# Kernel optimization log

Measured on AMD Instinct MI355X. Metric: run time of the kernel, lower is better.

## Reference

```python
import jax, jax.numpy as jnp
import numpy as np

B, D, E, K = 8192, 1024, 8, 2048  # tokens, dim, num_experts, k (per-expert capacity)


def setup_inputs() -> dict:
    key = jax.random.key(0)
    ks = jax.random.split(key, 5)
    x = jax.random.normal(ks[0], (B, D), dtype=jnp.float32)
    Wr = jax.random.normal(ks[1], (D, E), dtype=jnp.float32) * 0.02
    br = jnp.zeros((E,), jnp.float32)
    W1 = jax.random.normal(ks[2], (E, D, 4 * D), dtype=jnp.float32) * 0.02
    b1 = jnp.zeros((E, 4 * D), jnp.float32)
    W2 = jax.random.normal(ks[3], (E, 4 * D, D), dtype=jnp.float32) * 0.02
    b2 = jnp.zeros((E, D), jnp.float32)
    return {"x": x, "Wr": Wr, "br": br, "W1": W1, "b1": b1, "W2": W2, "b2": b2}


def _dispatch_weights(x, Wr, br):
    # Expert-choice routing: softmax over experts per token, each expert picks top-K tokens.
    gate = jax.nn.softmax(x @ Wr + br, axis=-1)          # [B, E]
    vals, idx = jax.lax.top_k(gate.T, K)                 # [E, K] each
    w = jnp.zeros((x.shape[0], E), x.dtype)
    w = w.at[idx.reshape(-1), jnp.repeat(jnp.arange(E), K)].set(vals.reshape(-1))
    # torch source builds dispatch_weights via .tolist(), detaching it from autograd
    return jax.lax.stop_gradient(w)                      # [B, E]


def reference(x, Wr, br, W1, b1, W2, b2):
    w = _dispatch_weights(x, Wr, br)                     # [B, E]
    mask = (w > 0).astype(x.dtype)                       # [B, E]
    xm = x[None, :, :] * mask.T[:, :, None]              # [E, B, D] (dense masked input, as in source)
    h = jax.nn.relu(jnp.einsum('ebd,edh->ebh', xm, W1) + b1[:, None, :])   # [E, B, 4D]
    y = jnp.einsum('ebh,ehd->ebd', h, W2) + b2[:, None, :]                 # [E, B, D]
    out = jnp.einsum('ebd,be->bd', y, w)                 # weighted combine over experts
    return out
```

## Files before the change

kernel.cpp:

```cpp
#include <hip/hip_runtime.h>
#include <hip/hip_bf16.h>

#define BTOK 8192
#define DDIM 1024
#define NEXP 8
#define KCAP 2048
#define HDIM 4096
#define MB ((size_t)1048576)

typedef __attribute__((ext_vector_type(4))) float f32x4;
typedef __attribute__((ext_vector_type(8))) short bf16x8;

__device__ __forceinline__ unsigned short f2bf(float f) {
    union { float f; unsigned u; } v; v.f = f;
    unsigned r = v.u + 0x7fffu + ((v.u >> 16) & 1u);
    return (unsigned short)(r >> 16);
}

typedef __attribute__((address_space(3))) unsigned int lds_u32;
typedef __attribute__((address_space(1))) const unsigned int glb_u32;
__device__ __forceinline__ void gl_lds16(const void* g, void* l) {
    __builtin_amdgcn_global_load_lds((glb_u32*)g, (lds_u32*)l, 16, 0, 0);
}

__global__ __launch_bounds__(256) void router_kernel(
    const float* __restrict__ x, const float* __restrict__ Wr,
    const float* __restrict__ br, float* __restrict__ gateT,
    unsigned short* __restrict__ xb) {
    __shared__ float wr_s[NEXP][DDIM];
    int t = threadIdx.x;
    for (int i = t; i < NEXP * DDIM; i += 256) {
        int e = i >> 10, d = i & 1023;
        wr_s[e][d] = Wr[d * NEXP + e];
    }
    __syncthreads();
    int wid = t >> 6, lane = t & 63;
    int b = blockIdx.x * 4 + wid;
    const float4* xr = (const float4*)(x + (size_t)b * DDIM);
    float4 xv[4];
#pragma unroll
    for (int j = 0; j < 4; j++) xv[j] = xr[j * 64 + lane];
#pragma unroll
    for (int j = 0; j < 4; j++) {
        short4 s;
        s.x = (short)f2bf(xv[j].x); s.y = (short)f2bf(xv[j].y);
        s.z = (short)f2bf(xv[j].z); s.w = (short)f2bf(xv[j].w);
        *(short4*)(xb + (size_t)b * DDIM + (j * 64 + lane) * 4) = s;
    }
    double acc[NEXP];
#pragma unroll
    for (int e = 0; e < NEXP; e++) {
        double a = 0.0;
#pragma unroll
        for (int j = 0; j < 4; j++) {
            float4 wv = ((const float4*)&wr_s[e][0])[j * 64 + lane];
            a += (double)xv[j].x * wv.x + (double)xv[j].y * wv.y
               + (double)xv[j].z * wv.z + (double)xv[j].w * wv.w;
        }
#pragma unroll
        for (int s = 1; s < 64; s <<= 1) a += __shfl_xor(a, s, 64);
        acc[e] = a + (double)br[e];
    }
    if (lane == 0) {
        double mx = acc[0];
#pragma unroll
        for (int e = 1; e < NEXP; e++) mx = fmax(mx, acc[e]);
        double p[NEXP]; double ssum = 0.0;
#pragma unroll
        for (int e = 0; e < NEXP; e++) { p[e] = exp(acc[e] - mx); ssum += p[e]; }
        double inv = 1.0 / ssum;
#pragma unroll
        for (int e = 0; e < NEXP; e++) gateT[e * BTOK + b] = (float)(p[e] * inv);
    }
}

__global__ __launch_bounds__(256) void select_kernel(
    const float* __restrict__ gateT, unsigned* __restrict__ meta) {
    int e = blockIdx.x, t = threadIdx.x;
    const float* g = gateT + e * BTOK;
    __shared__ unsigned hist[256];
    __shared__ unsigned sh_prefix;
    __shared__ int sh_rem;
    if (t == 0) { sh_prefix = 0; sh_rem = KCAP; }
    __syncthreads();
    for (int pass = 0; pass < 4; pass++) {
        int shift = 24 - pass * 8;
        hist[t] = 0;
        __syncthreads();
        unsigned pfx = sh_prefix;
        for (int i = t; i < BTOK; i += 256) {
            unsigned key = __float_as_uint(g[i]);
            if (pass == 0 || (key >> (shift + 8)) == pfx)
                atomicAdd(&hist[(key >> shift) & 255u], 1u);
        }
        __syncthreads();
        if (t == 0) {
            int rem = sh_rem, cum = 0, d = 0;
            for (int dd = 255; dd >= 0; dd--) {
                cum += (int)hist[dd];
                if (cum >= rem) { d = dd; break; }
            }
            sh_rem = rem - (cum - (int)hist[d]);
            sh_prefix = (pfx << 8) | (unsigned)d;
        }
        __syncthreads();
    }
    unsigned cutoff = sh_prefix;
    int cnt = 0;
    for (int i = t; i < BTOK; i += 256)
        if (__float_as_uint(g[i]) > cutoff) cnt++;
    __shared__ int red[256];
    red[t] = cnt; __syncthreads();
    for (int s = 128; s > 0; s >>= 1) { if (t < s) red[t] += red[t + s]; __syncthreads(); }
    if (t == 0) { meta[e] = cutoff; meta[NEXP + e] = (unsigned)red[0]; }
}

__global__ __launch_bounds__(256) void build_kernel(
    const float* __restrict__ gateT, const unsigned* __restrict__ meta,
    unsigned* __restrict__ cnt, int* __restrict__ idx_list, float* __restrict__ wt_list) {
    int e = blockIdx.y;
    int b = blockIdx.x * 256 + threadIdx.x;
    float gv = gateT[(size_t)e * BTOK + b];
    if (__float_as_uint(gv) > meta[e]) {
        unsigned pos = atomicAdd(&cnt[e], 1u);
        if (pos < KCAP) {
            idx_list[(size_t)e * KCAP + pos] = b;
            wt_list[(size_t)e * KCAP + pos] = gv;
        }
    }
}

__global__ __launch_bounds__(256) void tie_kernel(
    const float* __restrict__ gateT, const unsigned* __restrict__ meta,
    unsigned* __restrict__ cnt, int* __restrict__ idx_list, float* __restrict__ wt_list) {
    int e = blockIdx.x, t = threadIdx.x;
    unsigned cutoff = meta[e];
    int need = KCAP - (int)meta[NEXP + e];
    const float* g = gateT + (size_t)e * BTOK;
    __shared__ int pre[256];
    int base = t * 32;
    int c = 0;
    for (int j = 0; j < 32; j++) c += (__float_as_uint(g[base + j]) == cutoff) ? 1 : 0;
    pre[t] = c;
    __syncthreads();
    for (int s = 1; s < 256; s <<= 1) {
        int v = (t >= s) ? pre[t - s] : 0;
        __syncthreads();
        pre[t] += v;
        __syncthreads();
    }
    int rank = pre[t] - c;
    for (int j = 0; j < 32; j++) {
        float gv = g[base + j];
        if (__float_as_uint(gv) == cutoff) {
            if (rank < need) {
                unsigned pos = atomicAdd(&cnt[e], 1u);
                if (pos < KCAP) {
                    idx_list[(size_t)e * KCAP + pos] = base + j;
                    wt_list[(size_t)e * KCAP + pos] = gv;
                }
            }
            rank++;
        }
    }
}

__global__ __launch_bounds__(256) void invb_kernel(
    const int* __restrict__ idx_list, int* __restrict__ inv) {
    int i = blockIdx.x * 256 + threadIdx.x;
    int e = i >> 11, slot = i & (KCAP - 1);
    inv[(size_t)e * BTOK + idx_list[i]] = slot;
}

__global__ __launch_bounds__(256) void tcvt_kernel(
    const float* __restrict__ src, unsigned short* __restrict__ dst, int R, int C) {
    size_t zoff = (size_t)blockIdx.z * R * C;
    src += zoff; dst += zoff;
    __shared__ unsigned short tile[64][72];
    int c0 = blockIdx.x * 64, r0 = blockIdx.y * 64;
    int t = threadIdx.x;
    int cq = t & 15, rr = t >> 4;
#pragma unroll
    for (int ri = 0; ri < 4; ri++) {
        int r = ri * 16 + rr;
        float4 v = *(const float4*)(src + (size_t)(r0 + r) * C + c0 + cq * 4);
        tile[cq * 4 + 0][r] = f2bf(v.x);
        tile[cq * 4 + 1][r] = f2bf(v.y);
        tile[cq * 4 + 2][r] = f2bf(v.z);
        tile[cq * 4 + 3][r] = f2bf(v.w);
    }
    __syncthreads();
    int rq = t & 15, cc = t >> 4;
#pragma unroll
    for (int ci = 0; ci < 4; ci++) {
        int c = ci * 16 + cc;
        *(short4*)(dst + (size_t)(c0 + c) * R + r0 + rq * 4) = *(const short4*)&tile[c][rq * 4];
    }
}


#define ASLOT 4096
#define BSLOT 8192

__global__ __launch_bounds__(512, 4) void gemm1_kernel(
    const unsigned short* __restrict__ xb, const unsigned short* __restrict__ w1t,
    const float* __restrict__ b1, const int* __restrict__ idx_list,
    unsigned short* __restrict__ h) {
    int bid = blockIdx.x;
    int e = bid & 7, idx = bid >> 3;
    int m0 = (idx & 15) * 128, n0 = (idx >> 4) * 256;
    w1t      += (size_t)e * DDIM * HDIM;
    b1       += (size_t)e * HDIM;
    idx_list += (size_t)e * KCAP;
    h        += (size_t)e * KCAP * HDIM;
    __shared__ unsigned short As[3 * ASLOT];
    __shared__ unsigned short Bs[3 * BSLOT];
    __shared__ int toks[128];
    int t = threadIdx.x;
    if (t < 128) toks[t] = idx_list[m0 + t];
    __syncthreads();
    int w = t >> 6, lane = t & 63, l4 = lane >> 2;
    unsigned swz = (unsigned)(((lane & 3) ^ ((lane >> 3) & 3)) << 4);
    const char* pa  = (const char*)(xb + (size_t)toks[w * 16 + l4] * DDIM) + swz;
    const char* pb0 = (const char*)(w1t + (size_t)(n0 + w * 16 + l4) * DDIM) + swz;
    const char* pb1 = (const char*)(w1t + (size_t)(n0 + 128 + w * 16 + l4) * DDIM) + swz;
    unsigned short* da  = As + (w * 16) * 32;
    unsigned short* db0 = Bs + (w * 16) * 32;
    unsigned short* db1 = Bs + (128 + w * 16) * 32;
#define ST1(slot, koff) do {                                         \
    gl_lds16(pa  + (koff), da  + (slot) * ASLOT);                    \
    gl_lds16(pb0 + (koff), db0 + (slot) * BSLOT);                    \
    gl_lds16(pb1 + (koff), db1 + (slot) * BSLOT); } while (0)
    int wm = w >> 2, wn = w & 3;
    int fr = lane & 15, kg = lane >> 4;
    unsigned koffr = (unsigned)((kg ^ ((fr >> 1) & 3)) << 4);
    const int NT = DDIM / 32;
    f32x4 acc[4][4] = {};
    ST1(0, 0); ST1(1, 64);
    asm volatile("s_waitcnt vmcnt(3)" ::: "memory");
    __builtin_amdgcn_s_barrier();
    size_t ko = 128;
    int sw = 2, sr = 0;
    for (int kt = 0; kt < NT; kt++) {
        if (kt + 2 < NT) { ST1(sw, ko); ko += 64; }
        const char* ab = (const char*)As + sr * (ASLOT * 2);
        const char* bb = (const char*)Bs + sr * (BSLOT * 2);
        bf16x8 af[4], bf[4];
#pragma unroll
        for (int mf = 0; mf < 4; mf++)
            af[mf] = *(const bf16x8*)(ab + (wm * 64 + mf * 16 + fr) * 64 + koffr);
#pragma unroll
        for (int nf = 0; nf < 4; nf++)
            bf[nf] = *(const bf16x8*)(bb + (wn * 64 + nf * 16 + fr) * 64 + koffr);
        __builtin_amdgcn_s_setprio(1);
#pragma unroll
        for (int mf = 0; mf < 4; mf++)
#pragma unroll
            for (int nf = 0; nf < 4; nf++)
                acc[mf][nf] = __builtin_amdgcn_mfma_f32_16x16x32_bf16(
                    af[mf], bf[nf], acc[mf][nf], 0, 0, 0);
        __builtin_amdgcn_s_setprio(0);
        if (kt + 1 < NT) {
            if (kt + 2 < NT) asm volatile("s_waitcnt vmcnt(3)" ::: "memory");
            else             asm volatile("s_waitcnt vmcnt(0)" ::: "memory");
            __builtin_amdgcn_s_barrier();
        }
        sw = (sw == 2) ? 0 : sw + 1;
        sr = (sr == 2) ? 0 : sr + 1;
    }
#undef ST1
    int hi = lane >> 4;
#pragma unroll
    for (int nf = 0; nf < 4; nf++) {
        int col = n0 + wn * 64 + nf * 16 + fr;
        float bias = b1[col];
#pragma unroll
        for (int mf = 0; mf < 4; mf++) {
            int r0 = wm * 64 + mf * 16 + hi * 4;
#pragma unroll
            for (int r = 0; r < 4; r++) {
                float v = fmaxf(acc[mf][nf][r] + bias, 0.f);
                h[(size_t)(m0 + r0 + r) * HDIM + col] = f2bf(v);
            }
        }
    }
}

__global__ __launch_bounds__(512, 4) void gemm2y_kernel(
    const unsigned short* __restrict__ h, const unsigned short* __restrict__ w2t,
    const float* __restrict__ b2, const float* __restrict__ wt_list,
    float* __restrict__ yb) {
    int bid = blockIdx.x;
    int e = bid & 7, idx = bid >> 3;
    int m0 = (idx & 15) * 128, n0 = (idx >> 4) * 256;
    h       += (size_t)e * KCAP * HDIM;
    w2t     += (size_t)e * DDIM * HDIM;
    b2      += (size_t)e * DDIM;
    wt_list += (size_t)e * KCAP;
    yb      += (size_t)e * KCAP * DDIM;
    __shared__ unsigned short As[3 * ASLOT];
    __shared__ unsigned short Bs[3 * BSLOT];
    __shared__ float wts[128];
    int t = threadIdx.x;
    if (t < 128) wts[t] = wt_list[m0 + t];
    __syncthreads();
    int w = t >> 6, lane = t & 63, l4 = lane >> 2;
    unsigned swz = (unsigned)(((lane & 3) ^ ((lane >> 3) & 3)) << 4);
    const char* pa  = (const char*)(h + (size_t)(m0 + w * 16 + l4) * HDIM) + swz;
    const char* pb0 = (const char*)(w2t + (size_t)(n0 + w * 16 + l4) * HDIM) + swz;
    const char* pb1 = (const char*)(w2t + (size_t)(n0 + 128 + w * 16 + l4) * HDIM) + swz;
    unsigned short* da  = As + (w * 16) * 32;
    unsigned short* db0 = Bs + (w * 16) * 32;
    unsigned short* db1 = Bs + (128 + w * 16) * 32;
#define ST2(slot, koff) do {                                         \
    gl_lds16(pa  + (koff), da  + (slot) * ASLOT);                    \
    gl_lds16(pb0 + (koff), db0 + (slot) * BSLOT);                    \
    gl_lds16(pb1 + (koff), db1 + (slot) * BSLOT); } while (0)
    int wm = w >> 2, wn = w & 3;
    int fr = lane & 15, kg = lane >> 4;
    unsigned koffr = (unsigned)((kg ^ ((fr >> 1) & 3)) << 4);
    const int NT = HDIM / 32;
    f32x4 acc[4][4] = {};
    ST2(0, 0); ST2(1, 64);
    asm volatile("s_waitcnt vmcnt(3)" ::: "memory");
    __builtin_amdgcn_s_barrier();
    size_t ko = 128;
    int sw = 2, sr = 0;
    for (int kt = 0; kt < NT; kt++) {
        if (kt + 2 < NT) { ST2(sw, ko); ko += 64; }
        const char* ab = (const char*)As + sr * (ASLOT * 2);
        const char* bb = (const char*)Bs + sr * (BSLOT * 2);
        bf16x8 af[4], bf[4];
#pragma unroll
        for (int mf = 0; mf < 4; mf++)
            af[mf] = *(const bf16x8*)(ab + (wm * 64 + mf * 16 + fr) * 64 + koffr);
#pragma unroll
        for (int nf = 0; nf < 4; nf++)
            bf[nf] = *(const bf16x8*)(bb + (wn * 64 + nf * 16 + fr) * 64 + koffr);
        __builtin_amdgcn_s_setprio(1);
#pragma unroll
        for (int mf = 0; mf < 4; mf++)
#pragma unroll
            for (int nf = 0; nf < 4; nf++)
                acc[mf][nf] = __builtin_amdgcn_mfma_f32_16x16x32_bf16(
                    af[mf], bf[nf], acc[mf][nf], 0, 0, 0);
        __builtin_amdgcn_s_setprio(0);
        if (kt + 1 < NT) {
            if (kt + 2 < NT) asm volatile("s_waitcnt vmcnt(3)" ::: "memory");
            else             asm volatile("s_waitcnt vmcnt(0)" ::: "memory");
            __builtin_amdgcn_s_barrier();
        }
        sw = (sw == 2) ? 0 : sw + 1;
        sr = (sr == 2) ? 0 : sr + 1;
    }
#undef ST2
    int hi = lane >> 4;
#pragma unroll
    for (int nf = 0; nf < 4; nf++) {
        int col = n0 + wn * 64 + nf * 16 + fr;
        float bias = b2[col];
#pragma unroll
        for (int mf = 0; mf < 4; mf++) {
            int r0 = wm * 64 + mf * 16 + hi * 4;
#pragma unroll
            for (int r = 0; r < 4; r++) {
                int lrow = r0 + r;
                yb[(size_t)(m0 + lrow) * DDIM + col] = wts[lrow] * (acc[mf][nf][r] + bias);
            }
        }
    }
}

__global__ __launch_bounds__(256) void combine_kernel(
    const float* __restrict__ yb, const int* __restrict__ inv,
    float* __restrict__ out) {
    int b = blockIdx.x, t = threadIdx.x;
    float4 acc = {0.f, 0.f, 0.f, 0.f};
#pragma unroll
    for (int e = 0; e < NEXP; e++) {
        int s = inv[(size_t)e * BTOK + b];
        if (s >= 0) {
            float4 v = *(const float4*)(yb + ((size_t)e * KCAP + s) * DDIM + t * 4);
            acc.x += v.x; acc.y += v.y; acc.z += v.z; acc.w += v.w;
        }
    }
    *(float4*)(out + (size_t)b * DDIM + t * 4) = acc;
}

extern "C" void kernel_launch(void* const* d_in, const int* in_sizes, int n_in,
                              void* d_out, int out_size, void* d_ws, size_t ws_size,
                              hipStream_t stream) {
    const float* x  = (const float*)d_in[0];
    const float* Wr = (const float*)d_in[1];
    const float* br = (const float*)d_in[2];
    const float* W1 = (const float*)d_in[3];
    const float* b1 = (const float*)d_in[4];
    const float* W2 = (const float*)d_in[5];
    const float* b2 = (const float*)d_in[6];
    float* out = (float*)d_out;

    char* ws = (char*)d_ws;
    float*    gateT    = (float*)ws;
    unsigned* meta     = (unsigned*)(ws + 262144);
    unsigned* cnt      = meta + 16;
    int*      idx_list = (int*)(ws + 327680);
    float*    wt_list  = (float*)(ws + 393216);
    int*      inv      = (int*)(ws + 458752);
    unsigned short* xbuf = (unsigned short*)(ws + 1 * MB);
    unsigned short* w1t  = (unsigned short*)(ws + 17 * MB);
    unsigned short* w2t  = (unsigned short*)(ws + 81 * MB);
    unsigned short* hbuf = (unsigned short*)(ws + 145 * MB);
    float*          yb   = (float*)(ws + 273 * MB);
    const size_t NEED = 337 * MB;
    if (ws_size < NEED) return;

    hipMemsetAsync(cnt, 0, NEXP * sizeof(unsigned), stream);
    hipMemsetAsync(inv, 0xFF, (size_t)NEXP * BTOK * sizeof(int), stream);

    router_kernel<<<dim3(BTOK / 4), 256, 0, stream>>>(x, Wr, br, gateT, xbuf);
    select_kernel<<<dim3(NEXP), 256, 0, stream>>>(gateT, meta);
    build_kernel<<<dim3(BTOK / 256, NEXP), 256, 0, stream>>>(gateT, meta, cnt, idx_list, wt_list);
    tie_kernel<<<dim3(NEXP), 256, 0, stream>>>(gateT, meta, cnt, idx_list, wt_list);

    tcvt_kernel<<<dim3(HDIM / 64, DDIM / 64, NEXP), 256, 0, stream>>>(W1, w1t, DDIM, HDIM);
    tcvt_kernel<<<dim3(DDIM / 64, HDIM / 64, NEXP), 256, 0, stream>>>(W2, w2t, HDIM, DDIM);
    invb_kernel<<<dim3(NEXP * KCAP / 256), 256, 0, stream>>>(idx_list, inv);

    gemm1_kernel<<<dim3((KCAP / 128) * (HDIM / 256) * NEXP), 512, 0, stream>>>(
        xbuf, w1t, b1, idx_list, hbuf);
    gemm2y_kernel<<<dim3((KCAP / 128) * (DDIM / 256) * NEXP), 512, 0, stream>>>(
        hbuf, w2t, b2, wt_list, yb);
    combine_kernel<<<dim3(BTOK), 256, 0, stream>>>(yb, inv, out);
}
```

Measured before the change: 567.5 us.

## Fuse routing kernels, merge weight transposes, double-buffer gemm1 for occupancy

Merges the select, build, tie and inverse-index kernels into one per-expert route kernel that picks the top-K tokens and writes idx, weight and inverse slot directly, dropping the meta and count buffers and one memset. Combines the two weight transpose-convert launches into a single launch. Changes gemm1 from a triple-buffered to a double-buffered LDS pipeline with a higher occupancy hint, trading prefetch depth for more resident blocks. The single-block-per-expert route kernel does all selection serially on 8 blocks, and the shallower pipeline may expose memory latency.

```diff
diff --git a/kernel.cpp b/kernel.cpp
--- a/kernel.cpp
+++ b/kernel.cpp
@@ -74,14 +74,17 @@
     }
 }
 
-__global__ __launch_bounds__(256) void select_kernel(
-    const float* __restrict__ gateT, unsigned* __restrict__ meta) {
+__global__ __launch_bounds__(256) void route_kernel(
+    const float* __restrict__ gateT, int* __restrict__ idx_list,
+    float* __restrict__ wt_list, int* __restrict__ inv) {
     int e = blockIdx.x, t = threadIdx.x;
-    const float* g = gateT + e * BTOK;
+    const float* g = gateT + (size_t)e * BTOK;
     __shared__ unsigned hist[256];
+    __shared__ int pre[256];
     __shared__ unsigned sh_prefix;
     __shared__ int sh_rem;
-    if (t == 0) { sh_prefix = 0; sh_rem = KCAP; }
+    __shared__ unsigned cnt_s;
+    if (t == 0) { sh_prefix = 0; sh_rem = KCAP; cnt_s = 0; }
     __syncthreads();
     for (int pass = 0; pass < 4; pass++) {
         int shift = 24 - pass * 8;
@@ -106,78 +109,53 @@
         __syncthreads();
     }
     unsigned cutoff = sh_prefix;
-    int cnt = 0;
-    for (int i = t; i < BTOK; i += 256)
-        if (__float_as_uint(g[i]) > cutoff) cnt++;
-    __shared__ int red[256];
-    red[t] = cnt; __syncthreads();
-    for (int s = 128; s > 0; s >>= 1) { if (t < s) red[t] += red[t + s]; __syncthreads(); }
-    if (t == 0) { meta[e] = cutoff; meta[NEXP + e] = (unsigned)red[0]; }
-}
-
-__global__ __launch_bounds__(256) void build_kernel(
-    const float* __restrict__ gateT, const unsigned* __restrict__ meta,
-    unsigned* __restrict__ cnt, int* __restrict__ idx_list, float* __restrict__ wt_list) {
-    int e = blockIdx.y;
-    int b = blockIdx.x * 256 + threadIdx.x;
-    float gv = gateT[(size_t)e * BTOK + b];
-    if (__float_as_uint(gv) > meta[e]) {
-        unsigned pos = atomicAdd(&cnt[e], 1u);
-        if (pos < KCAP) {
+    int base = t * 32;
+    int ngt_t = 0, tie_t = 0;
+    for (int j = 0; j < 32; j++) {
+        unsigned key = __float_as_uint(g[base + j]);
+        ngt_t += (key > cutoff) ? 1 : 0;
+        tie_t += (key == cutoff) ? 1 : 0;
+    }
+    hist[t] = (unsigned)ngt_t;
+    pre[t] = tie_t;
+    __syncthreads();
+    for (int s = 128; s > 0; s >>= 1) {
+        if (t < s) hist[t] += hist[t + s];
+        __syncthreads();
+    }
+    int need = KCAP - (int)hist[0];
+    for (int s = 1; s < 256; s <<= 1) {
+        int v = (t >= s) ? pre[t - s] : 0;
+        __syncthreads();
+        pre[t] += v;
+        __syncthreads();
+    }
+    int rank = pre[t] - tie_t;
+    for (int j = 0; j < 32; j++) {
+        int b = base + j;
+        float gv = g[b];
+        unsigned key = __float_as_uint(gv);
+        bool sel = (key > cutoff);
+        if (!sel && key == cutoff) { sel = (rank < need); rank++; }
+        if (sel) {
+            unsigned pos = atomicAdd(&cnt_s, 1u);
             idx_list[(size_t)e * KCAP + pos] = b;
             wt_list[(size_t)e * KCAP + pos] = gv;
-        }
-    }
-}
-
-__global__ __launch_bounds__(256) void tie_kernel(
-    const float* __restrict__ gateT, const unsigned* __restrict__ meta,
-    unsigned* __restrict__ cnt, int* __restrict__ idx_list, float* __restrict__ wt_list) {
-    int e = blockIdx.x, t = threadIdx.x;
-    unsigned cutoff = meta[e];
-    int need = KCAP - (int)meta[NEXP + e];
-    const float* g = gateT + (size_t)e * BTOK;
-    __shared__ int pre[256];
-    int base = t * 32;
-    int c = 0;
-    for (int j = 0; j < 32; j++) c += (__float_as_uint(g[base + j]) == cutoff) ? 1 : 0;
-    pre[t] = c;
-    __syncthreads();
-    for (int s = 1; s < 256; s <<= 1) {
-        int v = (t >= s) ? pre[t - s] : 0;
-        __syncthreads();
-        pre[t] += v;
-        __syncthreads();
-    }
-    int rank = pre[t] - c;
-    for (int j = 0; j < 32; j++) {
-        float gv = g[base + j];
-        if (__float_as_uint(gv) == cutoff) {
-            if (rank < need) {
-                unsigned pos = atomicAdd(&cnt[e], 1u);
-                if (pos < KCAP) {
-                    idx_list[(size_t)e * KCAP + pos] = base + j;
-                    wt_list[(size_t)e * KCAP + pos] = gv;
-                }
-            }
-            rank++;
-        }
-    }
-}
-
-__global__ __launch_bounds__(256) void invb_kernel(
-    const int* __restrict__ idx_list, int* __restrict__ inv) {
-    int i = blockIdx.x * 256 + threadIdx.x;
-    int e = i >> 11, slot = i & (KCAP - 1);
-    inv[(size_t)e * BTOK + idx_list[i]] = slot;
-}
-
-__global__ __launch_bounds__(256) void tcvt_kernel(
-    const float* __restrict__ src, unsigned short* __restrict__ dst, int R, int C) {
-    size_t zoff = (size_t)blockIdx.z * R * C;
-    src += zoff; dst += zoff;
+            inv[(size_t)e * BTOK + b] = (int)pos;
+        }
+    }
+}
+
+__global__ __launch_bounds__(256) void tcvt2_kernel(
+    const float* __restrict__ W1, const float* __restrict__ W2,
+    unsigned short* __restrict__ w1t, unsigned short* __restrict__ w2t) {
+    int z = blockIdx.y;
+    const float* src; unsigned short* dst; int R, C;
+    if (z < 8) { src = W1 + (size_t)z * DDIM * HDIM; dst = w1t + (size_t)z * DDIM * HDIM; R = DDIM; C = HDIM; }
+    else       { src = W2 + (size_t)(z - 8) * DDIM * HDIM; dst = w2t + (size_t)(z - 8) * DDIM * HDIM; R = HDIM; C = DDIM; }
+    int ntx = C >> 6;
+    int c0 = (blockIdx.x % ntx) * 64, r0 = (blockIdx.x / ntx) * 64;
     __shared__ unsigned short tile[64][72];
-    int c0 = blockIdx.x * 64, r0 = blockIdx.y * 64;
     int t = threadIdx.x;
     int cq = t & 15, rr = t >> 4;
 #pragma unroll
@@ -202,7 +180,7 @@
 #define ASLOT 4096
 #define BSLOT 8192
 
-__global__ __launch_bounds__(512, 4) void gemm1_kernel(
+__global__ __launch_bounds__(512, 6) void gemm1_kernel(
     const unsigned short* __restrict__ xb, const unsigned short* __restrict__ w1t,
     const float* __restrict__ b1, const int* __restrict__ idx_list,
     unsigned short* __restrict__ h) {
@@ -213,8 +191,8 @@
     b1       += (size_t)e * HDIM;
     idx_list += (size_t)e * KCAP;
     h        += (size_t)e * KCAP * HDIM;
-    __shared__ unsigned short As[3 * ASLOT];
-    __shared__ unsigned short Bs[3 * BSLOT];
+    __shared__ unsigned short As[2 * ASLOT];
+    __shared__ unsigned short Bs[2 * BSLOT];
     __shared__ int toks[128];
     int t = threadIdx.x;
     if (t < 128) toks[t] = idx_list[m0 + t];
@@ -236,15 +214,13 @@
     unsigned koffr = (unsigned)((kg ^ ((fr >> 1) & 3)) << 4);
     const int NT = DDIM / 32;
     f32x4 acc[4][4] = {};
-    ST1(0, 0); ST1(1, 64);
-    asm volatile("s_waitcnt vmcnt(3)" ::: "memory");
+    ST1(0, 0);
+    asm volatile("s_waitcnt vmcnt(0)" ::: "memory");
     __builtin_amdgcn_s_barrier();
-    size_t ko = 128;
-    int sw = 2, sr = 0;
     for (int kt = 0; kt < NT; kt++) {
-        if (kt + 2 < NT) { ST1(sw, ko); ko += 64; }
-        const char* ab = (const char*)As + sr * (ASLOT * 2);
-        const char* bb = (const char*)Bs + sr * (BSLOT * 2);
+        if (kt + 1 < NT) ST1((kt + 1) & 1, (size_t)(kt + 1) * 64);
+        const char* ab = (const char*)As + (kt & 1) * (ASLOT * 2);
+        const char* bb = (const char*)Bs + (kt & 1) * (BSLOT * 2);
         bf16x8 af[4], bf[4];
 #pragma unroll
         for (int mf = 0; mf < 4; mf++)
@@ -261,12 +237,9 @@
                     af[mf], bf[nf], acc[mf][nf], 0, 0, 0);
         __builtin_amdgcn_s_setprio(0);
         if (kt + 1 < NT) {
-            if (kt + 2 < NT) asm volatile("s_waitcnt vmcnt(3)" ::: "memory");
-            else             asm volatile("s_waitcnt vmcnt(0)" ::: "memory");
+            asm volatile("s_waitcnt vmcnt(0)" ::: "memory");
             __builtin_amdgcn_s_barrier();
         }
-        sw = (sw == 2) ? 0 : sw + 1;
-        sr = (sr == 2) ? 0 : sr + 1;
     }
 #undef ST1
     int hi = lane >> 4;
@@ -401,8 +374,6 @@
 
     char* ws = (char*)d_ws;
     float*    gateT    = (float*)ws;
-    unsigned* meta     = (unsigned*)(ws + 262144);
-    unsigned* cnt      = meta + 16;
     int*      idx_list = (int*)(ws + 327680);
     float*    wt_list  = (float*)(ws + 393216);
     int*      inv      = (int*)(ws + 458752);
@@ -414,17 +385,11 @@
     const size_t NEED = 337 * MB;
     if (ws_size < NEED) return;
 
-    hipMemsetAsync(cnt, 0, NEXP * sizeof(unsigned), stream);
     hipMemsetAsync(inv, 0xFF, (size_t)NEXP * BTOK * sizeof(int), stream);
 
     router_kernel<<<dim3(BTOK / 4), 256, 0, stream>>>(x, Wr, br, gateT, xbuf);
-    select_kernel<<<dim3(NEXP), 256, 0, stream>>>(gateT, meta);
-    build_kernel<<<dim3(BTOK / 256, NEXP), 256, 0, stream>>>(gateT, meta, cnt, idx_list, wt_list);
-    tie_kernel<<<dim3(NEXP), 256, 0, stream>>>(gateT, meta, cnt, idx_list, wt_list);
-
-    tcvt_kernel<<<dim3(HDIM / 64, DDIM / 64, NEXP), 256, 0, stream>>>(W1, w1t, DDIM, HDIM);
-    tcvt_kernel<<<dim3(DDIM / 64, HDIM / 64, NEXP), 256, 0, stream>>>(W2, w2t, HDIM, DDIM);
-    invb_kernel<<<dim3(NEXP * KCAP / 256), 256, 0, stream>>>(idx_list, inv);
+    route_kernel<<<dim3(NEXP), 256, 0, stream>>>(gateT, idx_list, wt_list, inv);
+    tcvt2_kernel<<<dim3(1024, 16), 256, 0, stream>>>(W1, W2, w1t, w2t);
 
     gemm1_kernel<<<dim3((KCAP / 128) * (HDIM / 256) * NEXP), 512, 0, stream>>>(
         xbuf, w1t, b1, idx_list, hbuf);
```

Result: slower. 1.440 ms (+153.8%).
